# Kernel optimization log

Hardware: AMD Instinct MI355X
Metric: run time of the kernel (lower is better)

The kernel has to match this reference:

```python
import jax, jax.numpy as jnp
import numpy as np

B, N, DM, H, C, DC = 4, 1024, 512, 8, 3, 16  # batch, nodes, node_dim, heads, manifold components, per-component dim
DK = DM // H


def setup_inputs() -> dict:
    key = jax.random.key(0)
    ks = jax.random.split(key, 8)

    def lin_w(k):
        return jax.random.normal(k, (DM, DM), jnp.float32) / np.sqrt(DM).astype(np.float32)

    return {
        "h": jax.random.normal(ks[0], (B, N, DM), jnp.float32),
        "x": jax.random.normal(ks[1], (B, N, C * DC), jnp.float32),
        "Wq": lin_w(ks[2]), "bq": jnp.zeros((DM,), jnp.float32),
        "Wk": lin_w(ks[3]), "bk": jnp.zeros((DM,), jnp.float32),
        "Wv": lin_w(ks[4]), "bv": jnp.zeros((DM,), jnp.float32),
        "Wo": lin_w(ks[5]), "bo": jnp.zeros((DM,), jnp.float32),
        "alpha": jnp.ones((H, C), jnp.float32),
        "log_sigma": jnp.zeros((H, C), jnp.float32),
    }


def reference(h, x, Wq, bq, Wk, bk, Wv, bv, Wo, bo, alpha, log_sigma):
    b, n, dm = h.shape
    hh, cc = alpha.shape
    dk = dm // hh
    scale = 1.0 / np.sqrt(dk).astype(np.float32)

    def to_heads(t, W, bias):
        return (t @ W.T + bias).reshape(b, n, hh, dk).transpose(0, 2, 1, 3)  # (B,H,N,dk)

    Q = to_heads(h, Wq, bq)
    K = to_heads(h, Wk, bk)
    V = to_heads(h, Wv, bv)

    attn = jnp.einsum('bhid,bhjd->bhij', Q, K) * scale  # (B,H,N,N)

    # Geodesic kernel: per-component Euclidean distances on the product manifold.
    xs = x.reshape(b, n, cc, -1)                      # (B,N,C,dc)
    sq = jnp.sum(xs * xs, axis=-1)                    # (B,N,C)
    inner = jnp.einsum('bicd,bjcd->bijc', xs, xs)     # (B,N,N,C)
    d_sq = jnp.maximum(sq[:, :, None, :] + sq[:, None, :, :] - 2.0 * inner, 0.0)  # (B,N,N,C)

    sigma = jnp.clip(jnp.exp(log_sigma), 1e-4)        # (H,C)
    # exp(-d_c^2 / (2 sigma_{h,c}^2)) -> (B,H,N,N,C), then weight by alpha and sum over c
    e = jnp.exp(-d_sq[:, None] / (2.0 * (sigma ** 2)[None, :, None, None, :])).astype(attn.dtype)
    attn = attn + jnp.einsum('hc,bhijc->bhij', alpha, e)

    p = jax.nn.softmax(attn, axis=-1)
    out = jnp.einsum('bhij,bhjd->bhid', p, V)         # (B,H,N,dk)
    out = out.transpose(0, 2, 1, 3).reshape(b, n, dm)
    return out @ Wo.T + bo
```

## Files before the change

### kernel.cpp

```cpp
#include <hip/hip_runtime.h>
#include <math.h>

typedef __bf16 bf16;
typedef __attribute__((ext_vector_type(8))) __bf16 bf16x8;
typedef __attribute__((ext_vector_type(4))) float f32x4;

#define LOG2E 1.44269504088896f
#define SCALE 0.125f

__device__ inline f32x4 mfma16(bf16x8 a, bf16x8 b, f32x4 c) {
    return __builtin_amdgcn_mfma_f32_16x16x32_bf16(a, b, c, 0, 0, 0);
}
__device__ inline unsigned short bfb(bf16 v) {
    union { bf16 b; unsigned short u; } z; z.b = v; return z.u;
}
__device__ inline bf16x8 cvt8(float4 v0, float4 v1) {
    bf16x8 o;
    o[0] = (bf16)v0.x; o[1] = (bf16)v0.y; o[2] = (bf16)v0.z; o[3] = (bf16)v0.w;
    o[4] = (bf16)v1.x; o[5] = (bf16)v1.y; o[6] = (bf16)v1.z; o[7] = (bf16)v1.w;
    return o;
}

__global__ __launch_bounds__(256) void prep_kernel(
        const float* __restrict__ h, const float* __restrict__ x,
        const float* __restrict__ Wq, const float* __restrict__ Wk,
        const float* __restrict__ Wv, const float* __restrict__ Wo,
        const float* __restrict__ bq, const float* __restrict__ bk,
        const float* __restrict__ bv,
        bf16* __restrict__ hb, bf16* __restrict__ wpack, bf16* __restrict__ wob,
        float* __restrict__ bqkv, bf16* __restrict__ xb,
        unsigned* __restrict__ spack) {
    int stride = gridDim.x * blockDim.x;
    int tid = blockIdx.x * blockDim.x + threadIdx.x;
    for (int i = tid; i < 262144; i += stride) {
        const float4* s = (const float4*)h + 2 * i;
        ((bf16x8*)hb)[i] = cvt8(s[0], s[1]);
    }
    for (int i = tid; i < 32768; i += stride) {
        const float4* sq = (const float4*)Wq + 2 * i;
        const float4* sk = (const float4*)Wk + 2 * i;
        const float4* sv = (const float4*)Wv + 2 * i;
        const float4* so = (const float4*)Wo + 2 * i;
        ((bf16x8*)wpack)[i]         = cvt8(sq[0], sq[1]);
        ((bf16x8*)wpack)[32768 + i] = cvt8(sk[0], sk[1]);
        ((bf16x8*)wpack)[65536 + i] = cvt8(sv[0], sv[1]);
        ((bf16x8*)wob)[i]           = cvt8(so[0], so[1]);
    }
    for (int i = tid; i < 24576; i += stride) {
        const float4* s = (const float4*)x + 2 * i;
        ((bf16x8*)xb)[i] = cvt8(s[0], s[1]);
    }
    for (int i = tid; i < 1536; i += stride)
        bqkv[i] = (i < 512) ? bq[i] : (i < 1024 ? bk[i - 512] : bv[i - 1024]);
    for (int i = tid; i < 4096 * 3; i += stride) {
        int row = i / 3, c = i - row * 3;
        float s = 0.0f;
        for (int k = 0; k < 16; k++) {
            float v = (float)(bf16)x[row * 48 + c * 16 + k];
            s += v * v;
        }
        s = -0.5f * s;
        bf16 sh = (bf16)s;
        bf16 sl = (bf16)(s - (float)sh);
        spack[i] = (unsigned)bfb(sh) | ((unsigned)bfb(sl) << 16);
    }
}

__global__ __launch_bounds__(256) void gemm_qkv_kernel(
        const bf16* __restrict__ A, const bf16* __restrict__ Bm,
        const float* __restrict__ bias,
        bf16* __restrict__ Qb, bf16* __restrict__ Kb, bf16* __restrict__ Vt) {
    __shared__ bf16 smem[2 * 128 * 72];
    bf16 (*Asm)[72] = (bf16(*)[72])smem;
    bf16 (*Bsm)[72] = (bf16(*)[72])(smem + 128 * 72);
    int t = threadIdx.x, w = t >> 6, lane = t & 63, g = lane >> 4, lo = lane & 15;
    int rowbase = blockIdx.x * 128, colbase = blockIdx.y * 128;
    int wr = (w >> 1) * 64, wc = (w & 1) * 64;
    f32x4 acc[4][4] = {};
    int srow = t >> 2, scol = (t & 3) * 16;
    for (int kb = 0; kb < 512; kb += 64) {
        __syncthreads();
        for (int half = 0; half < 2; half++) {
            int r = srow + 64 * half;
            *(bf16x8*)&Asm[r][scol]     = *(const bf16x8*)&A[(size_t)(rowbase + r) * 512 + kb + scol];
            *(bf16x8*)&Asm[r][scol + 8] = *(const bf16x8*)&A[(size_t)(rowbase + r) * 512 + kb + scol + 8];
            *(bf16x8*)&Bsm[r][scol]     = *(const bf16x8*)&Bm[(size_t)(colbase + r) * 512 + kb + scol];
            *(bf16x8*)&Bsm[r][scol + 8] = *(const bf16x8*)&Bm[(size_t)(colbase + r) * 512 + kb + scol + 8];
        }
        __syncthreads();
        for (int kk = 0; kk < 64; kk += 32) {
            bf16x8 af[4], bfr[4];
            for (int m = 0; m < 4; m++) af[m]  = *(const bf16x8*)&Asm[wr + 16 * m + lo][kk + 8 * g];
            for (int n = 0; n < 4; n++) bfr[n] = *(const bf16x8*)&Bsm[wc + 16 * n + lo][kk + 8 * g];
            for (int m = 0; m < 4; m++)
                for (int n = 0; n < 4; n++)
                    acc[m][n] = mfma16(af[m], bfr[n], acc[m][n]);
        }
    }
    __syncthreads();
    bf16 (*Cl)[132] = (bf16(*)[132])smem;
    for (int n = 0; n < 4; n++) {
        float bv = bias[colbase + wc + 16 * n + lo];
        for (int m = 0; m < 4; m++)
            for (int r = 0; r < 4; r++)
                Cl[wr + 16 * m + 4 * g + r][wc + 16 * n + lo] = (bf16)(acc[m][n][r] + bv);
    }
    __syncthreads();
    int proj = colbase >> 9, h0 = (colbase >> 6) & 7;
    int bidx = rowbase >> 10, i0g = rowbase & 1023;
    if (proj < 2) {
        int row = t >> 1, half = t & 1;
        bf16* dst = (proj == 0 ? Qb : Kb) +
                    ((size_t)(bidx * 8 + h0 + half) * 1024 + i0g + row) * 64;
        for (int ch = 0; ch < 8; ch++)
            *(bf16x8*)&dst[ch * 8] = *(const bf16x8*)&Cl[row][half * 64 + ch * 8];
    } else {
        int dcol = t >> 1, ihalf = t & 1;
        int head = h0 + (dcol >> 6), d = dcol & 63;
        bf16* dst = Vt + ((size_t)(bidx * 8 + head) * 64 + d) * 1024 + i0g + ihalf * 64;
        for (int ch = 0; ch < 8; ch++) {
            bf16x8 v;
            for (int q = 0; q < 8; q++) v[q] = Cl[ihalf * 64 + ch * 8 + q][dcol];
            *(bf16x8*)&dst[ch * 8] = v;
        }
    }
}

__global__ __launch_bounds__(256) void attn_kernel(
        const bf16* __restrict__ Qb, const bf16* __restrict__ Kb,
        const bf16* __restrict__ Vt, const bf16* __restrict__ xb,
        const unsigned* __restrict__ spack,
        const float* __restrict__ alpha, const float* __restrict__ log_sigma,
        bf16* __restrict__ attnout) {
    __shared__ bf16 Klds[64][72];
    __shared__ bf16 VTlds[64][72];
    __shared__ bf16 Xlds[64][104];
    __shared__ bf16 Plds[4][16][72];

    int t = threadIdx.x;
    int w = t >> 6, lane = t & 63, g = lane >> 4, lo = lane & 15;
    int b = blockIdx.z;
    int hh = blockIdx.y;
    int i0 = blockIdx.x * 64 + w * 16;

    const unsigned ONE2 = 0x3F803F80u;
    float c1 = SCALE * LOG2E;
    float k2[3], alf[3];
    for (int c = 0; c < 3; c++) {
        float sg = fmaxf(expf(log_sigma[hh * 3 + c]), 1e-4f);
        k2[c] = LOG2E / (sg * sg);
        alf[c] = alpha[hh * 3 + c] * LOG2E;
    }

    const bf16* Qbase = Qb + ((size_t)(b * 8 + hh) * 1024 + i0) * 64;
    bf16x8 qa[2];
    qa[0] = *(const bf16x8*)&Qbase[lo * 64 + 8 * g];
    qa[1] = *(const bf16x8*)&Qbase[lo * 64 + 32 + 8 * g];

    bf16x8 xqa[3];
    for (int c = 0; c < 3; c++) {
        bf16x8 v = {};
        if (g < 2) {
            v = *(const bf16x8*)&xb[((size_t)(b << 10) + i0 + lo) * 48 + c * 16 + 8 * g];
        } else if (g == 2) {
            uint2 ap;
            ap.x = spack[((size_t)(b << 10) + i0 + lo) * 3 + c];
            ap.y = ONE2;
            ((uint2*)&v)[0] = ap;
        }
        xqa[c] = v;
    }

    bf16x8 ones;
    for (int e = 0; e < 8; e++) ones[e] = (bf16)1.0f;
    f32x4 o[4] = {};
    f32x4 lacc = {};

    for (int idx = t; idx < 1664; idx += 256)
        ((unsigned long long*)&Xlds[0][0])[idx] = 0ULL;

    int sr = t >> 2, sc = (t & 3) * 16;
    for (int j0 = 0; j0 < 1024; j0 += 64) {
        __syncthreads();
        const bf16* Kbase = Kb + ((size_t)(b * 8 + hh) * 1024 + j0) * 64;
        *(bf16x8*)&Klds[sr][sc]     = *(const bf16x8*)&Kbase[sr * 64 + sc];
        *(bf16x8*)&Klds[sr][sc + 8] = *(const bf16x8*)&Kbase[sr * 64 + sc + 8];
        const bf16* Vbase = Vt + ((size_t)(b * 8 + hh) * 64) * 1024 + j0;
        *(bf16x8*)&VTlds[sr][sc]     = *(const bf16x8*)&Vbase[sr * 1024 + sc];
        *(bf16x8*)&VTlds[sr][sc + 8] = *(const bf16x8*)&Vbase[sr * 1024 + sc + 8];
        if (t < 192) {
            int xr = t / 3, c = t - xr * 3;
            const bf16* xsrc = &xb[((size_t)(b << 10) + j0 + xr) * 48 + c * 16];
            *(bf16x8*)&Xlds[xr][c * 32]     = *(const bf16x8*)&xsrc[0];
            *(bf16x8*)&Xlds[xr][c * 32 + 8] = *(const bf16x8*)&xsrc[8];
            uint2 bp;
            bp.x = ONE2;
            bp.y = spack[((size_t)(b << 10) + j0 + xr) * 3 + c];
            *(uint2*)&Xlds[xr][c * 32 + 16] = bp;
        }
        __syncthreads();

        for (int tt = 0; tt < 4; tt++) {
            f32x4 acc = {};
            bf16x8 kb0 = *(const bf16x8*)&Klds[16 * tt + lo][8 * g];
            bf16x8 kb1 = *(const bf16x8*)&Klds[16 * tt + lo][32 + 8 * g];
            acc = mfma16(qa[0], kb0, acc);
            acc = mfma16(qa[1], kb1, acc);
            f32x4 z0 = {}, z1 = {}, z2 = {};
            f32x4 e0 = mfma16(xqa[0], *(const bf16x8*)&Xlds[16 * tt + lo][8 * g], z0);
            f32x4 e1 = mfma16(xqa[1], *(const bf16x8*)&Xlds[16 * tt + lo][32 + 8 * g], z1);
            f32x4 e2 = mfma16(xqa[2], *(const bf16x8*)&Xlds[16 * tt + lo][64 + 8 * g], z2);
            for (int r = 0; r < 4; r++) {
                float t0 = alf[0] * exp2f(k2[0] * fminf(e0[r], 0.0f));
                t0 = fmaf(alf[1], exp2f(k2[1] * fminf(e1[r], 0.0f)), t0);
                t0 = fmaf(alf[2], exp2f(k2[2] * fminf(e2[r], 0.0f)), t0);
                float p = exp2f(fmaf(acc[r], c1, t0));
                Plds[w][4 * g + r][16 * tt + lo] = (bf16)p;
            }
        }

        bf16x8 pa0 = *(const bf16x8*)&Plds[w][lo][8 * g];
        bf16x8 pa1 = *(const bf16x8*)&Plds[w][lo][32 + 8 * g];
        lacc = mfma16(pa0, ones, lacc);
        lacc = mfma16(pa1, ones, lacc);
        for (int td = 0; td < 4; td++) {
            bf16x8 vb0 = *(const bf16x8*)&VTlds[16 * td + lo][8 * g];
            bf16x8 vb1 = *(const bf16x8*)&VTlds[16 * td + lo][32 + 8 * g];
            o[td] = mfma16(pa0, vb0, o[td]);
            o[td] = mfma16(pa1, vb1, o[td]);
        }
    }

    float inv[4];
    for (int r = 0; r < 4; r++) inv[r] = 1.0f / lacc[r];
    for (int td = 0; td < 4; td++)
        for (int r = 0; r < 4; r++) {
            int i = i0 + 4 * g + r;
            attnout[((size_t)(b << 10) + i) * 512 + hh * 64 + 16 * td + lo] =
                (bf16)(o[td][r] * inv[r]);
        }
}

__global__ __launch_bounds__(256) void gemm_out_kernel(
        const bf16* __restrict__ A, const bf16* __restrict__ Bm,
        const float* __restrict__ bias, float* __restrict__ out) {
    __shared__ bf16 Asm[64][72];
    __shared__ bf16 Bsm[128][72];
    int t = threadIdx.x, w = t >> 6, lane = t & 63, g = lane >> 4, lo = lane & 15;
    int rowbase = blockIdx.x * 64, colbase = blockIdx.y * 128;
    int wr = (w >> 1) * 32, wc = (w & 1) * 64;
    f32x4 acc[2][4] = {};
    int arow = t >> 2, acol = (t & 3) * 16;
    int brow = t >> 1, bcol = (t & 1) * 32;
    for (int kb = 0; kb < 512; kb += 64) {
        __syncthreads();
        *(bf16x8*)&Asm[arow][acol]     = *(const bf16x8*)&A[(size_t)(rowbase + arow) * 512 + kb + acol];
        *(bf16x8*)&Asm[arow][acol + 8] = *(const bf16x8*)&A[(size_t)(rowbase + arow) * 512 + kb + acol + 8];
        *(bf16x8*)&Bsm[brow][bcol]      = *(const bf16x8*)&Bm[(size_t)(colbase + brow) * 512 + kb + bcol];
        *(bf16x8*)&Bsm[brow][bcol + 8]  = *(const bf16x8*)&Bm[(size_t)(colbase + brow) * 512 + kb + bcol + 8];
        *(bf16x8*)&Bsm[brow][bcol + 16] = *(const bf16x8*)&Bm[(size_t)(colbase + brow) * 512 + kb + bcol + 16];
        *(bf16x8*)&Bsm[brow][bcol + 24] = *(const bf16x8*)&Bm[(size_t)(colbase + brow) * 512 + kb + bcol + 24];
        __syncthreads();
        for (int kk = 0; kk < 64; kk += 32) {
            bf16x8 af[2], bfr[4];
            for (int m = 0; m < 2; m++) af[m]  = *(const bf16x8*)&Asm[wr + 16 * m + lo][kk + 8 * g];
            for (int n = 0; n < 4; n++) bfr[n] = *(const bf16x8*)&Bsm[wc + 16 * n + lo][kk + 8 * g];
            for (int m = 0; m < 2; m++)
                for (int n = 0; n < 4; n++)
                    acc[m][n] = mfma16(af[m], bfr[n], acc[m][n]);
        }
    }
    for (int n = 0; n < 4; n++) {
        int mcol = colbase + wc + 16 * n + lo;
        float bv = bias[mcol];
        for (int m = 0; m < 2; m++)
            for (int r = 0; r < 4; r++)
                out[(size_t)(rowbase + wr + 16 * m + 4 * g + r) * 512 + mcol] =
                    acc[m][n][r] + bv;
    }
}

extern "C" void kernel_launch(void* const* d_in, const int* in_sizes, int n_in,
                              void* d_out, int out_size, void* d_ws, size_t ws_size,
                              hipStream_t stream) {
    const float* h  = (const float*)d_in[0];
    const float* x  = (const float*)d_in[1];
    const float* Wq = (const float*)d_in[2];
    const float* bq = (const float*)d_in[3];
    const float* Wk = (const float*)d_in[4];
    const float* bk = (const float*)d_in[5];
    const float* Wv = (const float*)d_in[6];
    const float* bv = (const float*)d_in[7];
    const float* Wo = (const float*)d_in[8];
    const float* bo = (const float*)d_in[9];
    const float* alpha     = (const float*)d_in[10];
    const float* log_sigma = (const float*)d_in[11];
    float* out = (float*)d_out;

    char* ws = (char*)d_ws;
    size_t off = 0;
    auto alloc = [&](size_t bytes) {
        char* p = ws + off;
        off += (bytes + 255) & ~(size_t)255;
        return p;
    };
    bf16*     hb      = (bf16*)alloc(4096 * 512 * 2);
    bf16*     wpack   = (bf16*)alloc(1536 * 512 * 2);
    bf16*     wob     = (bf16*)alloc(512 * 512 * 2);
    float*    bqkv    = (float*)alloc(1536 * 4);
    bf16*     xb      = (bf16*)alloc(4096 * 48 * 2);
    unsigned* spack   = (unsigned*)alloc((size_t)4096 * 3 * 4);
    bf16*     Qb      = (bf16*)alloc((size_t)4 * 8 * 1024 * 64 * 2);
    bf16*     Kb      = (bf16*)alloc((size_t)4 * 8 * 1024 * 64 * 2);
    bf16*     Vt      = (bf16*)alloc((size_t)4 * 8 * 1024 * 64 * 2);
    bf16*     attnout = (bf16*)alloc(4096 * 512 * 2);

    prep_kernel<<<512, 256, 0, stream>>>(h, x, Wq, Wk, Wv, Wo, bq, bk, bv,
                                         hb, wpack, wob, bqkv, xb, spack);
    gemm_qkv_kernel<<<dim3(32, 12), 256, 0, stream>>>(hb, wpack, bqkv, Qb, Kb, Vt);
    attn_kernel<<<dim3(16, 8, 4), 256, 0, stream>>>(
        Qb, Kb, Vt, xb, spack, alpha, log_sigma, attnout);
    gemm_out_kernel<<<dim3(64, 4), 256, 0, stream>>>(attnout, wob, bo, out);
}
```

Baseline: 171.3 us.

## Fuse fp32-to-bf16 prep into GEMMs and split attention KV range in two

Removes the separate prep kernel. The h/W/x conversion to bf16 and the squared-norm computation now happen inside the QKV GEMM and attention tile loads. Attention is split along the key dimension into two halves, doubling the grid. Unnormalized fp32 partial outputs and row sums go to the workspace and are combined, normalized and cast to bf16 in the output GEMM's A-tile load. This saves one launch and the intermediate bf16 round trip and improves occupancy, at the cost of repeated fp32 weight reads and conversions per tile and extra fp32 partial-output traffic.

```diff
diff --git a/kernel.cpp b/kernel.cpp
--- a/kernel.cpp
+++ b/kernel.cpp
@@ -10,9 +10,6 @@
 
 __device__ inline f32x4 mfma16(bf16x8 a, bf16x8 b, f32x4 c) {
     return __builtin_amdgcn_mfma_f32_16x16x32_bf16(a, b, c, 0, 0, 0);
-}
-__device__ inline unsigned short bfb(bf16 v) {
-    union { bf16 b; unsigned short u; } z; z.b = v; return z.u;
 }
 __device__ inline bf16x8 cvt8(float4 v0, float4 v1) {
     bf16x8 o;
@@ -21,60 +18,20 @@
     return o;
 }
 
-__global__ __launch_bounds__(256) void prep_kernel(
-        const float* __restrict__ h, const float* __restrict__ x,
-        const float* __restrict__ Wq, const float* __restrict__ Wk,
-        const float* __restrict__ Wv, const float* __restrict__ Wo,
+__global__ __launch_bounds__(256) void gemm_qkv_kernel(
+        const float* __restrict__ A, const float* __restrict__ Wq,
+        const float* __restrict__ Wk, const float* __restrict__ Wv,
         const float* __restrict__ bq, const float* __restrict__ bk,
         const float* __restrict__ bv,
-        bf16* __restrict__ hb, bf16* __restrict__ wpack, bf16* __restrict__ wob,
-        float* __restrict__ bqkv, bf16* __restrict__ xb,
-        unsigned* __restrict__ spack) {
-    int stride = gridDim.x * blockDim.x;
-    int tid = blockIdx.x * blockDim.x + threadIdx.x;
-    for (int i = tid; i < 262144; i += stride) {
-        const float4* s = (const float4*)h + 2 * i;
-        ((bf16x8*)hb)[i] = cvt8(s[0], s[1]);
-    }
-    for (int i = tid; i < 32768; i += stride) {
-        const float4* sq = (const float4*)Wq + 2 * i;
-        const float4* sk = (const float4*)Wk + 2 * i;
-        const float4* sv = (const float4*)Wv + 2 * i;
-        const float4* so = (const float4*)Wo + 2 * i;
-        ((bf16x8*)wpack)[i]         = cvt8(sq[0], sq[1]);
-        ((bf16x8*)wpack)[32768 + i] = cvt8(sk[0], sk[1]);
-        ((bf16x8*)wpack)[65536 + i] = cvt8(sv[0], sv[1]);
-        ((bf16x8*)wob)[i]           = cvt8(so[0], so[1]);
-    }
-    for (int i = tid; i < 24576; i += stride) {
-        const float4* s = (const float4*)x + 2 * i;
-        ((bf16x8*)xb)[i] = cvt8(s[0], s[1]);
-    }
-    for (int i = tid; i < 1536; i += stride)
-        bqkv[i] = (i < 512) ? bq[i] : (i < 1024 ? bk[i - 512] : bv[i - 1024]);
-    for (int i = tid; i < 4096 * 3; i += stride) {
-        int row = i / 3, c = i - row * 3;
-        float s = 0.0f;
-        for (int k = 0; k < 16; k++) {
-            float v = (float)(bf16)x[row * 48 + c * 16 + k];
-            s += v * v;
-        }
-        s = -0.5f * s;
-        bf16 sh = (bf16)s;
-        bf16 sl = (bf16)(s - (float)sh);
-        spack[i] = (unsigned)bfb(sh) | ((unsigned)bfb(sl) << 16);
-    }
-}
-
-__global__ __launch_bounds__(256) void gemm_qkv_kernel(
-        const bf16* __restrict__ A, const bf16* __restrict__ Bm,
-        const float* __restrict__ bias,
         bf16* __restrict__ Qb, bf16* __restrict__ Kb, bf16* __restrict__ Vt) {
     __shared__ bf16 smem[2 * 128 * 72];
     bf16 (*Asm)[72] = (bf16(*)[72])smem;
     bf16 (*Bsm)[72] = (bf16(*)[72])(smem + 128 * 72);
     int t = threadIdx.x, w = t >> 6, lane = t & 63, g = lane >> 4, lo = lane & 15;
     int rowbase = blockIdx.x * 128, colbase = blockIdx.y * 128;
+    int proj = colbase >> 9, wcol = colbase & 511;
+    const float* Wsrc = (proj == 0) ? Wq : (proj == 1 ? Wk : Wv);
+    const float* bsrc = (proj == 0) ? bq : (proj == 1 ? bk : bv);
     int wr = (w >> 1) * 64, wc = (w & 1) * 64;
     f32x4 acc[4][4] = {};
     int srow = t >> 2, scol = (t & 3) * 16;
@@ -82,10 +39,12 @@
         __syncthreads();
         for (int half = 0; half < 2; half++) {
             int r = srow + 64 * half;
-            *(bf16x8*)&Asm[r][scol]     = *(const bf16x8*)&A[(size_t)(rowbase + r) * 512 + kb + scol];
-            *(bf16x8*)&Asm[r][scol + 8] = *(const bf16x8*)&A[(size_t)(rowbase + r) * 512 + kb + scol + 8];
-            *(bf16x8*)&Bsm[r][scol]     = *(const bf16x8*)&Bm[(size_t)(colbase + r) * 512 + kb + scol];
-            *(bf16x8*)&Bsm[r][scol + 8] = *(const bf16x8*)&Bm[(size_t)(colbase + r) * 512 + kb + scol + 8];
+            const float4* as = (const float4*)&A[(size_t)(rowbase + r) * 512 + kb + scol];
+            *(bf16x8*)&Asm[r][scol]     = cvt8(as[0], as[1]);
+            *(bf16x8*)&Asm[r][scol + 8] = cvt8(as[2], as[3]);
+            const float4* bs = (const float4*)&Wsrc[(size_t)(wcol + r) * 512 + kb + scol];
+            *(bf16x8*)&Bsm[r][scol]     = cvt8(bs[0], bs[1]);
+            *(bf16x8*)&Bsm[r][scol + 8] = cvt8(bs[2], bs[3]);
         }
         __syncthreads();
         for (int kk = 0; kk < 64; kk += 32) {
@@ -100,13 +59,13 @@
     __syncthreads();
     bf16 (*Cl)[132] = (bf16(*)[132])smem;
     for (int n = 0; n < 4; n++) {
-        float bv = bias[colbase + wc + 16 * n + lo];
+        float bv = bsrc[wcol + wc + 16 * n + lo];
         for (int m = 0; m < 4; m++)
             for (int r = 0; r < 4; r++)
                 Cl[wr + 16 * m + 4 * g + r][wc + 16 * n + lo] = (bf16)(acc[m][n][r] + bv);
     }
     __syncthreads();
-    int proj = colbase >> 9, h0 = (colbase >> 6) & 7;
+    int h0 = (colbase >> 6) & 7;
     int bidx = rowbase >> 10, i0g = rowbase & 1023;
     if (proj < 2) {
         int row = t >> 1, half = t & 1;
@@ -128,22 +87,21 @@
 
 __global__ __launch_bounds__(256) void attn_kernel(
         const bf16* __restrict__ Qb, const bf16* __restrict__ Kb,
-        const bf16* __restrict__ Vt, const bf16* __restrict__ xb,
-        const unsigned* __restrict__ spack,
+        const bf16* __restrict__ Vt, const float* __restrict__ x,
         const float* __restrict__ alpha, const float* __restrict__ log_sigma,
-        bf16* __restrict__ attnout) {
+        float* __restrict__ o_part, float* __restrict__ l_part) {
     __shared__ bf16 Klds[64][72];
     __shared__ bf16 VTlds[64][72];
-    __shared__ bf16 Xlds[64][104];
+    __shared__ bf16 Xlds[64][80];
     __shared__ bf16 Plds[4][16][72];
 
     int t = threadIdx.x;
     int w = t >> 6, lane = t & 63, g = lane >> 4, lo = lane & 15;
-    int b = blockIdx.z;
+    int zz = blockIdx.z;
+    int b = zz >> 1, split = zz & 1;
     int hh = blockIdx.y;
     int i0 = blockIdx.x * 64 + w * 16;
 
-    const unsigned ONE2 = 0x3F803F80u;
     float c1 = SCALE * LOG2E;
     float k2[3], alf[3];
     for (int c = 0; c < 3; c++) {
@@ -161,12 +119,21 @@
     for (int c = 0; c < 3; c++) {
         bf16x8 v = {};
         if (g < 2) {
-            v = *(const bf16x8*)&xb[((size_t)(b << 10) + i0 + lo) * 48 + c * 16 + 8 * g];
+            const float4* xs = (const float4*)&x[((size_t)(b << 10) + i0 + lo) * 48 + c * 16 + 8 * g];
+            v = cvt8(xs[0], xs[1]);
         } else if (g == 2) {
-            uint2 ap;
-            ap.x = spack[((size_t)(b << 10) + i0 + lo) * 3 + c];
-            ap.y = ONE2;
-            ((uint2*)&v)[0] = ap;
+            const float* xr = &x[((size_t)(b << 10) + i0 + lo) * 48 + c * 16];
+            float s = 0.0f;
+            for (int k = 0; k < 16; k++) {
+                float vv = (float)(bf16)xr[k];
+                s += vv * vv;
+            }
+            s = -0.5f * s;
+            bf16 sh = (bf16)s;
+            v[0] = sh;
+            v[1] = (bf16)(s - (float)sh);
+            v[2] = (bf16)1.0f;
+            v[3] = (bf16)1.0f;
         }
         xqa[c] = v;
     }
@@ -176,11 +143,12 @@
     f32x4 o[4] = {};
     f32x4 lacc = {};
 
-    for (int idx = t; idx < 1664; idx += 256)
-        ((unsigned long long*)&Xlds[0][0])[idx] = 0ULL;
+    for (int idx = t; idx < 64; idx += 256)
+        *(uint4*)&Xlds[idx][72] = (uint4){0, 0, 0, 0};
 
     int sr = t >> 2, sc = (t & 3) * 16;
-    for (int j0 = 0; j0 < 1024; j0 += 64) {
+    int jb = split * 512;
+    for (int j0 = jb; j0 < jb + 512; j0 += 64) {
         __syncthreads();
         const bf16* Kbase = Kb + ((size_t)(b * 8 + hh) * 1024 + j0) * 64;
         *(bf16x8*)&Klds[sr][sc]     = *(const bf16x8*)&Kbase[sr * 64 + sc];
@@ -190,13 +158,24 @@
         *(bf16x8*)&VTlds[sr][sc + 8] = *(const bf16x8*)&Vbase[sr * 1024 + sc + 8];
         if (t < 192) {
             int xr = t / 3, c = t - xr * 3;
-            const bf16* xsrc = &xb[((size_t)(b << 10) + j0 + xr) * 48 + c * 16];
-            *(bf16x8*)&Xlds[xr][c * 32]     = *(const bf16x8*)&xsrc[0];
-            *(bf16x8*)&Xlds[xr][c * 32 + 8] = *(const bf16x8*)&xsrc[8];
-            uint2 bp;
-            bp.x = ONE2;
-            bp.y = spack[((size_t)(b << 10) + j0 + xr) * 3 + c];
-            *(uint2*)&Xlds[xr][c * 32 + 16] = bp;
+            const float4* xs = (const float4*)&x[((size_t)(b << 10) + j0 + xr) * 48 + c * 16];
+            bf16x8 d0 = cvt8(xs[0], xs[1]);
+            bf16x8 d1 = cvt8(xs[2], xs[3]);
+            *(bf16x8*)&Xlds[xr][c * 24]     = d0;
+            *(bf16x8*)&Xlds[xr][c * 24 + 8] = d1;
+            float s = 0.0f;
+            for (int k = 0; k < 8; k++) {
+                float a0 = (float)d0[k], a1 = (float)d1[k];
+                s += a0 * a0 + a1 * a1;
+            }
+            s = -0.5f * s;
+            bf16 sh = (bf16)s;
+            bf16x8 cst = {};
+            cst[0] = (bf16)1.0f;
+            cst[1] = (bf16)1.0f;
+            cst[2] = sh;
+            cst[3] = (bf16)(s - (float)sh);
+            *(bf16x8*)&Xlds[xr][c * 24 + 16] = cst;
         }
         __syncthreads();
 
@@ -208,8 +187,8 @@
             acc = mfma16(qa[1], kb1, acc);
             f32x4 z0 = {}, z1 = {}, z2 = {};
             f32x4 e0 = mfma16(xqa[0], *(const bf16x8*)&Xlds[16 * tt + lo][8 * g], z0);
-            f32x4 e1 = mfma16(xqa[1], *(const bf16x8*)&Xlds[16 * tt + lo][32 + 8 * g], z1);
-            f32x4 e2 = mfma16(xqa[2], *(const bf16x8*)&Xlds[16 * tt + lo][64 + 8 * g], z2);
+            f32x4 e1 = mfma16(xqa[1], *(const bf16x8*)&Xlds[16 * tt + lo][24 + 8 * g], z1);
+            f32x4 e2 = mfma16(xqa[2], *(const bf16x8*)&Xlds[16 * tt + lo][48 + 8 * g], z2);
             for (int r = 0; r < 4; r++) {
                 float t0 = alf[0] * exp2f(k2[0] * fminf(e0[r], 0.0f));
                 t0 = fmaf(alf[1], exp2f(k2[1] * fminf(e1[r], 0.0f)), t0);
@@ -231,19 +210,22 @@
         }
     }
 
-    float inv[4];
-    for (int r = 0; r < 4; r++) inv[r] = 1.0f / lacc[r];
     for (int td = 0; td < 4; td++)
         for (int r = 0; r < 4; r++) {
-            int i = i0 + 4 * g + r;
-            attnout[((size_t)(b << 10) + i) * 512 + hh * 64 + 16 * td + lo] =
-                (bf16)(o[td][r] * inv[r]);
+            size_t rowg = (size_t)(b * 8 + hh) * 1024 + i0 + 4 * g + r;
+            o_part[((size_t)split * 32768 + rowg) * 64 + 16 * td + lo] = o[td][r];
+        }
+    if (lo == 0)
+        for (int r = 0; r < 4; r++) {
+            size_t rowg = (size_t)(b * 8 + hh) * 1024 + i0 + 4 * g + r;
+            l_part[(size_t)split * 32768 + rowg] = lacc[r];
         }
 }
 
 __global__ __launch_bounds__(256) void gemm_out_kernel(
-        const bf16* __restrict__ A, const bf16* __restrict__ Bm,
-        const float* __restrict__ bias, float* __restrict__ out) {
+        const float* __restrict__ o_part, const float* __restrict__ l_part,
+        const float* __restrict__ Wo, const float* __restrict__ bo,
+        float* __restrict__ out) {
     __shared__ bf16 Asm[64][72];
     __shared__ bf16 Bsm[128][72];
     int t = threadIdx.x, w = t >> 6, lane = t & 63, g = lane >> 4, lo = lane & 15;
@@ -254,12 +236,36 @@
     int brow = t >> 1, bcol = (t & 1) * 32;
     for (int kb = 0; kb < 512; kb += 64) {
         __syncthreads();
-        *(bf16x8*)&Asm[arow][acol]     = *(const bf16x8*)&A[(size_t)(rowbase + arow) * 512 + kb + acol];
-        *(bf16x8*)&Asm[arow][acol + 8] = *(const bf16x8*)&A[(size_t)(rowbase + arow) * 512 + kb + acol + 8];
-        *(bf16x8*)&Bsm[brow][bcol]      = *(const bf16x8*)&Bm[(size_t)(colbase + brow) * 512 + kb + bcol];
-        *(bf16x8*)&Bsm[brow][bcol + 8]  = *(const bf16x8*)&Bm[(size_t)(colbase + brow) * 512 + kb + bcol + 8];
-        *(bf16x8*)&Bsm[brow][bcol + 16] = *(const bf16x8*)&Bm[(size_t)(colbase + brow) * 512 + kb + bcol + 16];
-        *(bf16x8*)&Bsm[brow][bcol + 24] = *(const bf16x8*)&Bm[(size_t)(colbase + brow) * 512 + kb + bcol + 24];
+        {
+            int hh = kb >> 6;
+            int n = rowbase + arow;
+            size_t rowg = (size_t)((n >> 10) * 8 + hh) * 1024 + (n & 1023);
+            const float* p0 = &o_part[rowg * 64 + acol];
+            const float* p1 = &o_part[((size_t)32768 + rowg) * 64 + acol];
+            float inv = 1.0f / (l_part[rowg] + l_part[32768 + rowg]);
+            float4 a0 = ((const float4*)p0)[0], a1 = ((const float4*)p0)[1];
+            float4 a2 = ((const float4*)p0)[2], a3 = ((const float4*)p0)[3];
+            float4 c0 = ((const float4*)p1)[0], c1 = ((const float4*)p1)[1];
+            float4 c2 = ((const float4*)p1)[2], c3 = ((const float4*)p1)[3];
+            bf16x8 r0, r1;
+            r0[0] = (bf16)((a0.x + c0.x) * inv); r0[1] = (bf16)((a0.y + c0.y) * inv);
+            r0[2] = (bf16)((a0.z + c0.z) * inv); r0[3] = (bf16)((a0.w + c0.w) * inv);
+            r0[4] = (bf16)((a1.x + c1.x) * inv); r0[5] = (bf16)((a1.y + c1.y) * inv);
+            r0[6] = (bf16)((a1.z + c1.z) * inv); r0[7] = (bf16)((a1.w + c1.w) * inv);
+            r1[0] = (bf16)((a2.x + c2.x) * inv); r1[1] = (bf16)((a2.y + c2.y) * inv);
+            r1[2] = (bf16)((a2.z + c2.z) * inv); r1[3] = (bf16)((a2.w + c2.w) * inv);
+            r1[4] = (bf16)((a3.x + c3.x) * inv); r1[5] = (bf16)((a3.y + c3.y) * inv);
+            r1[6] = (bf16)((a3.z + c3.z) * inv); r1[7] = (bf16)((a3.w + c3.w) * inv);
+            *(bf16x8*)&Asm[arow][acol]     = r0;
+            *(bf16x8*)&Asm[arow][acol + 8] = r1;
+        }
+        {
+            const float4* bs = (const float4*)&Wo[(size_t)(colbase + brow) * 512 + kb + bcol];
+            *(bf16x8*)&Bsm[brow][bcol]      = cvt8(bs[0], bs[1]);
+            *(bf16x8*)&Bsm[brow][bcol + 8]  = cvt8(bs[2], bs[3]);
+            *(bf16x8*)&Bsm[brow][bcol + 16] = cvt8(bs[4], bs[5]);
+            *(bf16x8*)&Bsm[brow][bcol + 24] = cvt8(bs[6], bs[7]);
+        }
         __syncthreads();
         for (int kk = 0; kk < 64; kk += 32) {
             bf16x8 af[2], bfr[4];
@@ -272,7 +278,7 @@
     }
     for (int n = 0; n < 4; n++) {
         int mcol = colbase + wc + 16 * n + lo;
-        float bv = bias[mcol];
+        float bv = bo[mcol];
         for (int m = 0; m < 2; m++)
             for (int r = 0; r < 4; r++)
                 out[(size_t)(rowbase + wr + 16 * m + 4 * g + r) * 512 + mcol] =
@@ -304,21 +310,15 @@
         off += (bytes + 255) & ~(size_t)255;
         return p;
     };
-    bf16*     hb      = (bf16*)alloc(4096 * 512 * 2);
-    bf16*     wpack   = (bf16*)alloc(1536 * 512 * 2);
-    bf16*     wob     = (bf16*)alloc(512 * 512 * 2);
-    float*    bqkv    = (float*)alloc(1536 * 4);
-    bf16*     xb      = (bf16*)alloc(4096 * 48 * 2);
-    unsigned* spack   = (unsigned*)alloc((size_t)4096 * 3 * 4);
-    bf16*     Qb      = (bf16*)alloc((size_t)4 * 8 * 1024 * 64 * 2);
-    bf16*     Kb      = (bf16*)alloc((size_t)4 * 8 * 1024 * 64 * 2);
-    bf16*     Vt      = (bf16*)alloc((size_t)4 * 8 * 1024 * 64 * 2);
-    bf16*     attnout = (bf16*)alloc(4096 * 512 * 2);
-
-    prep_kernel<<<512, 256, 0, stream>>>(h, x, Wq, Wk, Wv, Wo, bq, bk, bv,
-                                         hb, wpack, wob, bqkv, xb, spack);
-    gemm_qkv_kernel<<<dim3(32, 12), 256, 0, stream>>>(hb, wpack, bqkv, Qb, Kb, Vt);
-    attn_kernel<<<dim3(16, 8, 4), 256, 0, stream>>>(
-        Qb, Kb, Vt, xb, spack, alpha, log_sigma, attnout);
-    gemm_out_kernel<<<dim3(64, 4), 256, 0, stream>>>(attnout, wob, bo, out);
-}
+    bf16*  Qb     = (bf16*)alloc((size_t)4 * 8 * 1024 * 64 * 2);
+    bf16*  Kb     = (bf16*)alloc((size_t)4 * 8 * 1024 * 64 * 2);
+    bf16*  Vt     = (bf16*)alloc((size_t)4 * 8 * 1024 * 64 * 2);
+    float* o_part = (float*)alloc((size_t)2 * 32768 * 64 * 4);
+    float* l_part = (float*)alloc((size_t)2 * 32768 * 4);
+
+    gemm_qkv_kernel<<<dim3(32, 12), 256, 0, stream>>>(h, Wq, Wk, Wv, bq, bk, bv,
+                                                      Qb, Kb, Vt);
+    attn_kernel<<<dim3(16, 8, 8), 256, 0, stream>>>(
+        Qb, Kb, Vt, x, alpha, log_sigma, o_part, l_part);
+    gemm_out_kernel<<<dim3(64, 4), 256, 0, stream>>>(o_part, l_part, Wo, bo, out);
+}
```

New measurement: 184.0 us. 7.4% more time.
